# Kernel optimization log

Measured on AMD Instinct MI355X. Metric: run time of the kernel, lower is better.

## Reference

```python
import jax, jax.numpy as jnp
import numpy as np

B, S, H, NREL = 4, 512, 256, 99


def setup_inputs() -> dict:
    key = jax.random.key(0)
    ks = jax.random.split(key, 6)
    return {
        "queries": jax.random.normal(ks[0], (B, S, H), dtype=jnp.float32),
        "keys": jax.random.normal(ks[1], (B, S, H), dtype=jnp.float32),
        "relations": jax.random.randint(ks[2], (B, S, S), 0, NREL, dtype=jnp.int64),
        "Wq": jax.random.normal(ks[3], (H, H), dtype=jnp.float32) * 0.02,
        "bq": jnp.zeros((H,), dtype=jnp.float32),
        "Wk": jax.random.normal(ks[4], (H, H), dtype=jnp.float32) * 0.02,
        "bk": jnp.zeros((H,), dtype=jnp.float32),
        "rel_emb": jax.random.normal(ks[5], (NREL, H), dtype=jnp.float32) * 0.02,
    }


def reference(queries, keys, relations, Wq, bq, Wk, bk, rel_emb):
    # Linear projections (torch Linear: x @ W.T + b)
    q = queries @ Wq.T + bq        # [B, Sq, H]
    k = keys @ Wk.T + bk           # [B, Sk, H]
    r = rel_emb[relations]         # [B, Sq, Sk, H]

    # single head: qk^T + q . r^T, scaled
    qk = jnp.einsum("bqd,bkd->bqk", q, k)       # [B, Sq, Sk]
    qr = jnp.einsum("bqd,bqkd->bqk", q, r)      # [B, Sq, Sk]
    scale = 1.0 / jnp.sqrt(jnp.asarray(q.shape[-1], q.dtype))
    logits = (qk + qr) * scale
    return jax.nn.softmax(logits, axis=-1)       # squeezed head dim -> [B, Sq, Sk]
```

## Files before the change

kernel.cpp:

```cpp
#include <hip/hip_runtime.h>

typedef __attribute__((ext_vector_type(8))) short bf8;
typedef __attribute__((ext_vector_type(4))) float f4;

#define QBF  0
#define KBF  524288
#define WQBF 1048576
#define WKBF 1114112
#define REBF 1179648

static __device__ __forceinline__ short bfr(float x) {
    union { float f; unsigned u; } v; v.f = x;
    return (short)((v.u + 0x7FFF + ((v.u >> 16) & 1)) >> 16);
}
static __device__ __forceinline__ bf8 pack8(float4 a, float4 b) {
    bf8 r;
    r[0] = bfr(a.x); r[1] = bfr(a.y); r[2] = bfr(a.z); r[3] = bfr(a.w);
    r[4] = bfr(b.x); r[5] = bfr(b.y); r[6] = bfr(b.z); r[7] = bfr(b.w);
    return r;
}

__global__ __launch_bounds__(256) void cast_kernel(const float* __restrict__ Wq,
                                                   const float* __restrict__ Wk,
                                                   const float* __restrict__ re,
                                                   short* __restrict__ ws) {
    int e8 = (blockIdx.x * 256 + threadIdx.x) * 8;
    float4 a = make_float4(0.f, 0.f, 0.f, 0.f), b = a;
    short* dst;
    if (e8 < 65536) {
        const float4* s = (const float4*)(Wq + e8);
        a = s[0]; b = s[1];
        dst = ws + WQBF + e8;
    } else if (e8 < 131072) {
        const float4* s = (const float4*)(Wk + (e8 - 65536));
        a = s[0]; b = s[1];
        dst = ws + WKBF + (e8 - 65536);
    } else {
        int idx = e8 - 131072;
        dst = ws + REBF + idx;
        if ((idx >> 8) < 99) {
            const float4* s = (const float4*)(re + idx);
            a = s[0]; b = s[1];
        }
    }
    *(bf8*)dst = pack8(a, b);
}

__global__ __launch_bounds__(512) void proj_kernel(const float* __restrict__ queries,
                                                   const float* __restrict__ keys,
                                                   const float* __restrict__ bq,
                                                   const float* __restrict__ bk,
                                                   short* __restrict__ ws) {
    int mat = blockIdx.x >> 6;
    int t = blockIdx.x & 63;
    int m0 = (t >> 2) * 128;
    int n0 = (t & 3) * 64;
    int w = threadIdx.x >> 6;
    int lane = threadIdx.x & 63;
    int n15 = lane & 15, quad = lane >> 4;

    const float* x = mat ? keys : queries;
    const short* wb = ws + (mat ? WKBF : WQBF);
    const float* bias = mat ? bk : bq;
    short* outp = ws + (mat ? KBF : QBF);

    int mrow = m0 + w * 16 + n15;
    bf8 afr[8];
#pragma unroll
    for (int kk = 0; kk < 8; kk++) {
        const float4* ap = (const float4*)(x + mrow * 256 + kk * 32 + quad * 8);
        afr[kk] = pack8(ap[0], ap[1]);
    }

    f4 z = {0.f, 0.f, 0.f, 0.f};
    f4 c[4] = {z, z, z, z};
#pragma unroll
    for (int nt = 0; nt < 4; nt++) {
        int col = n0 + nt * 16 + n15;
        const short* wr = wb + col * 256 + quad * 8;
#pragma unroll
        for (int kk = 0; kk < 8; kk++) {
            bf8 bfrag = *(const bf8*)(wr + kk * 32);
            c[nt] = __builtin_amdgcn_mfma_f32_16x16x32_bf16(afr[kk], bfrag, c[nt], 0, 0, 0);
        }
    }

    int mbase = m0 + w * 16 + quad * 4;
#pragma unroll
    for (int nt = 0; nt < 4; nt++) {
        int col = n0 + nt * 16 + n15;
        float bv = bias[col];
#pragma unroll
        for (int reg = 0; reg < 4; reg++)
            outp[(mbase + reg) * 256 + col] = bfr(c[nt][reg] + bv);
    }
}

__global__ __launch_bounds__(512) void attn_kernel(const int* __restrict__ relations,
                                                   const short* __restrict__ ws,
                                                   float* __restrict__ out) {
    __shared__ float qr_l[16][112];
    __shared__ float red_m[16][8];
    __shared__ float red_s[16][8];

    int b = blockIdx.x >> 5;
    int i0 = (blockIdx.x & 31) * 16;
    int gi0 = b * 512 + i0;
    int w = threadIdx.x >> 6;
    int lane = threadIdx.x & 63;
    int n15 = lane & 15, quad = lane >> 4;
    int j0 = w * 64;

    const int* rb = relations + (gi0 + quad * 4) * 512 + j0 + n15;
    int rv[4][4];
#pragma unroll
    for (int reg = 0; reg < 4; reg++)
#pragma unroll
        for (int nt = 0; nt < 4; nt++)
            rv[nt][reg] = rb[reg * 512 + nt * 16];

    const short* qbf = ws + QBF;
    const short* kbf = ws + KBF;
    const short* rebf = ws + REBF;

    int arow = gi0 + n15;
    bf8 afr[8];
#pragma unroll
    for (int kk = 0; kk < 8; kk++)
        afr[kk] = *(const bf8*)(qbf + arow * 256 + kk * 32 + quad * 8);

    f4 z = {0.f, 0.f, 0.f, 0.f};
    f4 c[4] = {z, z, z, z};
#pragma unroll
    for (int nt = 0; nt < 4; nt++) {
        int krow = b * 512 + j0 + nt * 16 + n15;
        const short* kr = kbf + krow * 256 + quad * 8;
#pragma unroll
        for (int kk = 0; kk < 8; kk++) {
            bf8 bfrag = *(const bf8*)(kr + kk * 32);
            c[nt] = __builtin_amdgcn_mfma_f32_16x16x32_bf16(afr[kk], bfrag, c[nt], 0, 0, 0);
        }
    }

    if (w < 7) {
        f4 cq = z;
        const short* rr = rebf + (w * 16 + n15) * 256 + quad * 8;
#pragma unroll
        for (int kk = 0; kk < 8; kk++) {
            bf8 bfrag = *(const bf8*)(rr + kk * 32);
            cq = __builtin_amdgcn_mfma_f32_16x16x32_bf16(afr[kk], bfrag, cq, 0, 0, 0);
        }
#pragma unroll
        for (int reg = 0; reg < 4; reg++)
            qr_l[quad * 4 + reg][w * 16 + n15] = cq[reg];
    }
    __syncthreads();

    const float scale = 0.0625f;
    float lg[4][4];
#pragma unroll
    for (int nt = 0; nt < 4; nt++)
#pragma unroll
        for (int reg = 0; reg < 4; reg++)
            lg[nt][reg] = (c[nt][reg] + qr_l[quad * 4 + reg][rv[nt][reg]]) * scale;

    float pm[4];
#pragma unroll
    for (int reg = 0; reg < 4; reg++) {
        float m = fmaxf(fmaxf(lg[0][reg], lg[1][reg]), fmaxf(lg[2][reg], lg[3][reg]));
#pragma unroll
        for (int d = 1; d <= 8; d <<= 1) m = fmaxf(m, __shfl_xor(m, d, 64));
        pm[reg] = m;
    }
    if (n15 == 0)
#pragma unroll
        for (int reg = 0; reg < 4; reg++) red_m[quad * 4 + reg][w] = pm[reg];
    __syncthreads();
    float M[4];
#pragma unroll
    for (int reg = 0; reg < 4; reg++) {
        f4 a0 = *(const f4*)&red_m[quad * 4 + reg][0];
        f4 a1 = *(const f4*)&red_m[quad * 4 + reg][4];
        M[reg] = fmaxf(fmaxf(fmaxf(a0[0], a0[1]), fmaxf(a0[2], a0[3])),
                       fmaxf(fmaxf(a1[0], a1[1]), fmaxf(a1[2], a1[3])));
    }

    float ps[4];
#pragma unroll
    for (int reg = 0; reg < 4; reg++) {
        float s = 0.f;
#pragma unroll
        for (int nt = 0; nt < 4; nt++) {
            float e = __expf(lg[nt][reg] - M[reg]);
            lg[nt][reg] = e;
            s += e;
        }
#pragma unroll
        for (int d = 1; d <= 8; d <<= 1) s += __shfl_xor(s, d, 64);
        ps[reg] = s;
    }
    if (n15 == 0)
#pragma unroll
        for (int reg = 0; reg < 4; reg++) red_s[quad * 4 + reg][w] = ps[reg];
    __syncthreads();
    float inv[4];
#pragma unroll
    for (int reg = 0; reg < 4; reg++) {
        f4 a0 = *(const f4*)&red_s[quad * 4 + reg][0];
        f4 a1 = *(const f4*)&red_s[quad * 4 + reg][4];
        inv[reg] = 1.f / (a0[0] + a0[1] + a0[2] + a0[3] + a1[0] + a1[1] + a1[2] + a1[3]);
    }

    float* ob = out + (gi0 + quad * 4) * 512 + j0 + n15;
#pragma unroll
    for (int reg = 0; reg < 4; reg++)
#pragma unroll
        for (int nt = 0; nt < 4; nt++)
            ob[reg * 512 + nt * 16] = lg[nt][reg] * inv[reg];
}

extern "C" void kernel_launch(void* const* d_in, const int* in_sizes, int n_in,
                              void* d_out, int out_size, void* d_ws, size_t ws_size,
                              hipStream_t stream) {
    const float* queries = (const float*)d_in[0];
    const float* keys = (const float*)d_in[1];
    const int* relations = (const int*)d_in[2];
    const float* Wq = (const float*)d_in[3];
    const float* bq = (const float*)d_in[4];
    const float* Wk = (const float*)d_in[5];
    const float* bk = (const float*)d_in[6];
    const float* rel_emb = (const float*)d_in[7];
    short* wss = (short*)d_ws;
    float* out = (float*)d_out;

    hipLaunchKernelGGL(cast_kernel, dim3(78), dim3(256), 0, stream, Wq, Wk, rel_emb, wss);
    hipLaunchKernelGGL(proj_kernel, dim3(128), dim3(512), 0, stream, queries, keys, bq, bk, wss);
    hipLaunchKernelGGL(attn_kernel, dim3(128), dim3(512), 0, stream, relations, wss, out);
}
```

Baseline: 99.82 us.

## Fuse cast, projection and attention into one cooperative kernel with grid sync

Merges the three launches into one cooperative kernel of 135 blocks. Blocks 0-127 convert their weight slice to bf16 straight into LDS and compute the Q/K projections, while blocks 128-134 convert the relation embeddings. After a grid-wide sync, the first 128 blocks run the attention and softmax. The relations index loads are issued before the projection so their latency overlaps it. This removes two kernel launch gaps and the round trip of the bf16 weights through global memory, at the cost of a grid barrier and cooperative launch overhead.

```diff
diff --git a/kernel.cpp b/kernel.cpp
--- a/kernel.cpp
+++ b/kernel.cpp
@@ -1,13 +1,14 @@
 #include <hip/hip_runtime.h>
+#include <hip/hip_cooperative_groups.h>
+
+namespace cg = cooperative_groups;
 
 typedef __attribute__((ext_vector_type(8))) short bf8;
 typedef __attribute__((ext_vector_type(4))) float f4;
 
 #define QBF  0
 #define KBF  524288
-#define WQBF 1048576
-#define WKBF 1114112
-#define REBF 1179648
+#define REBF 1048576
 
 static __device__ __forceinline__ short bfr(float x) {
     union { float f; unsigned u; } v; v.f = x;
@@ -20,104 +21,110 @@
     return r;
 }
 
-__global__ __launch_bounds__(256) void cast_kernel(const float* __restrict__ Wq,
-                                                   const float* __restrict__ Wk,
-                                                   const float* __restrict__ re,
-                                                   short* __restrict__ ws) {
-    int e8 = (blockIdx.x * 256 + threadIdx.x) * 8;
-    float4 a = make_float4(0.f, 0.f, 0.f, 0.f), b = a;
-    short* dst;
-    if (e8 < 65536) {
-        const float4* s = (const float4*)(Wq + e8);
-        a = s[0]; b = s[1];
-        dst = ws + WQBF + e8;
-    } else if (e8 < 131072) {
-        const float4* s = (const float4*)(Wk + (e8 - 65536));
-        a = s[0]; b = s[1];
-        dst = ws + WKBF + (e8 - 65536);
+__global__ __launch_bounds__(512) void fused_kernel(const int* __restrict__ relations,
+                                                    const float* __restrict__ queries,
+                                                    const float* __restrict__ keys,
+                                                    const float* __restrict__ bq,
+                                                    const float* __restrict__ bk,
+                                                    const float* __restrict__ Wq,
+                                                    const float* __restrict__ Wk,
+                                                    const float* __restrict__ rel_emb,
+                                                    short* __restrict__ ws,
+                                                    float* __restrict__ out) {
+    __shared__ union {
+        short w_l[64 * 264];
+        struct {
+            float qr[16][112];
+            float rm[16][8];
+            float rs[16][8];
+        } p1;
+    } sm;
+
+    cg::grid_group grid = cg::this_grid();
+
+    int blk = blockIdx.x;
+    int tid = threadIdx.x;
+    int w = tid >> 6;
+    int lane = tid & 63;
+    int n15 = lane & 15, quad = lane >> 4;
+
+    int rv[4][4];
+    if (blk < 128) {
+        int b_ = blk >> 5;
+        int i0_ = (blk & 31) * 16;
+        const int* rb = relations + ((b_ * 512 + i0_) + quad * 4) * 512 + w * 64 + n15;
+#pragma unroll
+        for (int reg = 0; reg < 4; reg++)
+#pragma unroll
+            for (int nt = 0; nt < 4; nt++)
+                rv[nt][reg] = rb[reg * 512 + nt * 16];
+    }
+
+    if (blk < 128) {
+        int mat = blk >> 6;
+        int t = blk & 63;
+        int m0 = (t >> 2) * 128;
+        int n0 = (t & 3) * 64;
+        const float* x = mat ? keys : queries;
+        const float* W = mat ? Wk : Wq;
+        const float* bias = mat ? bk : bq;
+        short* outp = ws + (mat ? KBF : QBF);
+
+#pragma unroll
+        for (int cc = 0; cc < 4; cc++) {
+            int chunk = cc * 512 + tid;
+            int row = chunk >> 5, col8 = chunk & 31;
+            const float4* s = (const float4*)(W + (n0 + row) * 256 + col8 * 8);
+            *(bf8*)&sm.w_l[row * 264 + col8 * 8] = pack8(s[0], s[1]);
+        }
+
+        int mrow = m0 + w * 16 + n15;
+        bf8 afr[8];
+#pragma unroll
+        for (int kk = 0; kk < 8; kk++) {
+            const float4* ap = (const float4*)(x + mrow * 256 + kk * 32 + quad * 8);
+            afr[kk] = pack8(ap[0], ap[1]);
+        }
+        __syncthreads();
+
+        f4 z = {0.f, 0.f, 0.f, 0.f};
+        f4 c[4] = {z, z, z, z};
+#pragma unroll
+        for (int nt = 0; nt < 4; nt++) {
+            const short* wr = &sm.w_l[(nt * 16 + n15) * 264 + quad * 8];
+#pragma unroll
+            for (int kk = 0; kk < 8; kk++) {
+                bf8 bfrag = *(const bf8*)(wr + kk * 32);
+                c[nt] = __builtin_amdgcn_mfma_f32_16x16x32_bf16(afr[kk], bfrag, c[nt], 0, 0, 0);
+            }
+        }
+
+        int mbase = m0 + w * 16 + quad * 4;
+#pragma unroll
+        for (int nt = 0; nt < 4; nt++) {
+            int col = n0 + nt * 16 + n15;
+            float bv = bias[col];
+#pragma unroll
+            for (int reg = 0; reg < 4; reg++)
+                outp[(mbase + reg) * 256 + col] = bfr(c[nt][reg] + bv);
+        }
     } else {
-        int idx = e8 - 131072;
-        dst = ws + REBF + idx;
-        if ((idx >> 8) < 99) {
-            const float4* s = (const float4*)(re + idx);
+        int idx8 = ((blk - 128) * 512 + tid) * 8;
+        float4 a = make_float4(0.f, 0.f, 0.f, 0.f), b = a;
+        if ((idx8 >> 8) < 99) {
+            const float4* s = (const float4*)(rel_emb + idx8);
             a = s[0]; b = s[1];
         }
-    }
-    *(bf8*)dst = pack8(a, b);
-}
-
-__global__ __launch_bounds__(512) void proj_kernel(const float* __restrict__ queries,
-                                                   const float* __restrict__ keys,
-                                                   const float* __restrict__ bq,
-                                                   const float* __restrict__ bk,
-                                                   short* __restrict__ ws) {
-    int mat = blockIdx.x >> 6;
-    int t = blockIdx.x & 63;
-    int m0 = (t >> 2) * 128;
-    int n0 = (t & 3) * 64;
-    int w = threadIdx.x >> 6;
-    int lane = threadIdx.x & 63;
-    int n15 = lane & 15, quad = lane >> 4;
-
-    const float* x = mat ? keys : queries;
-    const short* wb = ws + (mat ? WKBF : WQBF);
-    const float* bias = mat ? bk : bq;
-    short* outp = ws + (mat ? KBF : QBF);
-
-    int mrow = m0 + w * 16 + n15;
-    bf8 afr[8];
-#pragma unroll
-    for (int kk = 0; kk < 8; kk++) {
-        const float4* ap = (const float4*)(x + mrow * 256 + kk * 32 + quad * 8);
-        afr[kk] = pack8(ap[0], ap[1]);
-    }
-
-    f4 z = {0.f, 0.f, 0.f, 0.f};
-    f4 c[4] = {z, z, z, z};
-#pragma unroll
-    for (int nt = 0; nt < 4; nt++) {
-        int col = n0 + nt * 16 + n15;
-        const short* wr = wb + col * 256 + quad * 8;
-#pragma unroll
-        for (int kk = 0; kk < 8; kk++) {
-            bf8 bfrag = *(const bf8*)(wr + kk * 32);
-            c[nt] = __builtin_amdgcn_mfma_f32_16x16x32_bf16(afr[kk], bfrag, c[nt], 0, 0, 0);
-        }
-    }
-
-    int mbase = m0 + w * 16 + quad * 4;
-#pragma unroll
-    for (int nt = 0; nt < 4; nt++) {
-        int col = n0 + nt * 16 + n15;
-        float bv = bias[col];
-#pragma unroll
-        for (int reg = 0; reg < 4; reg++)
-            outp[(mbase + reg) * 256 + col] = bfr(c[nt][reg] + bv);
-    }
-}
-
-__global__ __launch_bounds__(512) void attn_kernel(const int* __restrict__ relations,
-                                                   const short* __restrict__ ws,
-                                                   float* __restrict__ out) {
-    __shared__ float qr_l[16][112];
-    __shared__ float red_m[16][8];
-    __shared__ float red_s[16][8];
-
-    int b = blockIdx.x >> 5;
-    int i0 = (blockIdx.x & 31) * 16;
+        *(bf8*)(ws + REBF + idx8) = pack8(a, b);
+    }
+
+    grid.sync();
+    if (blk >= 128) return;
+
+    int b = blk >> 5;
+    int i0 = (blk & 31) * 16;
     int gi0 = b * 512 + i0;
-    int w = threadIdx.x >> 6;
-    int lane = threadIdx.x & 63;
-    int n15 = lane & 15, quad = lane >> 4;
     int j0 = w * 64;
-
-    const int* rb = relations + (gi0 + quad * 4) * 512 + j0 + n15;
-    int rv[4][4];
-#pragma unroll
-    for (int reg = 0; reg < 4; reg++)
-#pragma unroll
-        for (int nt = 0; nt < 4; nt++)
-            rv[nt][reg] = rb[reg * 512 + nt * 16];
 
     const short* qbf = ws + QBF;
     const short* kbf = ws + KBF;
@@ -152,7 +159,7 @@
         }
 #pragma unroll
         for (int reg = 0; reg < 4; reg++)
-            qr_l[quad * 4 + reg][w * 16 + n15] = cq[reg];
+            sm.p1.qr[quad * 4 + reg][w * 16 + n15] = cq[reg];
     }
     __syncthreads();
 
@@ -162,7 +169,7 @@
     for (int nt = 0; nt < 4; nt++)
 #pragma unroll
         for (int reg = 0; reg < 4; reg++)
-            lg[nt][reg] = (c[nt][reg] + qr_l[quad * 4 + reg][rv[nt][reg]]) * scale;
+            lg[nt][reg] = (c[nt][reg] + sm.p1.qr[quad * 4 + reg][rv[nt][reg]]) * scale;
 
     float pm[4];
 #pragma unroll
@@ -174,13 +181,13 @@
     }
     if (n15 == 0)
 #pragma unroll
-        for (int reg = 0; reg < 4; reg++) red_m[quad * 4 + reg][w] = pm[reg];
+        for (int reg = 0; reg < 4; reg++) sm.p1.rm[quad * 4 + reg][w] = pm[reg];
     __syncthreads();
     float M[4];
 #pragma unroll
     for (int reg = 0; reg < 4; reg++) {
-        f4 a0 = *(const f4*)&red_m[quad * 4 + reg][0];
-        f4 a1 = *(const f4*)&red_m[quad * 4 + reg][4];
+        f4 a0 = *(const f4*)&sm.p1.rm[quad * 4 + reg][0];
+        f4 a1 = *(const f4*)&sm.p1.rm[quad * 4 + reg][4];
         M[reg] = fmaxf(fmaxf(fmaxf(a0[0], a0[1]), fmaxf(a0[2], a0[3])),
                        fmaxf(fmaxf(a1[0], a1[1]), fmaxf(a1[2], a1[3])));
     }
@@ -201,13 +208,13 @@
     }
     if (n15 == 0)
 #pragma unroll
-        for (int reg = 0; reg < 4; reg++) red_s[quad * 4 + reg][w] = ps[reg];
+        for (int reg = 0; reg < 4; reg++) sm.p1.rs[quad * 4 + reg][w] = ps[reg];
     __syncthreads();
     float inv[4];
 #pragma unroll
     for (int reg = 0; reg < 4; reg++) {
-        f4 a0 = *(const f4*)&red_s[quad * 4 + reg][0];
-        f4 a1 = *(const f4*)&red_s[quad * 4 + reg][4];
+        f4 a0 = *(const f4*)&sm.p1.rs[quad * 4 + reg][0];
+        f4 a1 = *(const f4*)&sm.p1.rs[quad * 4 + reg][4];
         inv[reg] = 1.f / (a0[0] + a0[1] + a0[2] + a0[3] + a1[0] + a1[1] + a1[2] + a1[3]);
     }
 
@@ -233,7 +240,8 @@
     short* wss = (short*)d_ws;
     float* out = (float*)d_out;
 
-    hipLaunchKernelGGL(cast_kernel, dim3(78), dim3(256), 0, stream, Wq, Wk, rel_emb, wss);
-    hipLaunchKernelGGL(proj_kernel, dim3(128), dim3(512), 0, stream, queries, keys, bq, bk, wss);
-    hipLaunchKernelGGL(attn_kernel, dim3(128), dim3(512), 0, stream, relations, wss, out);
-}
+    void* kargs[] = {(void*)&relations, (void*)&queries, (void*)&keys,
+                     (void*)&bq, (void*)&bk, (void*)&Wq, (void*)&Wk,
+                     (void*)&rel_emb, (void*)&wss, (void*)&out};
+    hipLaunchCooperativeKernel((void*)fused_kernel, dim3(135), dim3(512), kargs, 0, stream);
+}
```

After: 130.8 us. 31.0% more time.

## Fold weight casting into projection kernel and double attention grid parallelism

Applied to the files above, without the earlier changes.

Removes the separate cast kernel: projection blocks now load and convert their weight tile to bf16 in shared memory, and extra blocks cast rel_emb. The projection grid grows to 256 smaller-row tiles, and the attention kernel processes 8 query rows per block (256 blocks) with duplicated MFMA rows, writing only half. This cuts one launch and spreads work over more CUs, at the cost of redundant MFMA work and repeated weight conversion per block.

```diff
diff --git a/kernel.cpp b/kernel.cpp
--- a/kernel.cpp
+++ b/kernel.cpp
@@ -5,9 +5,7 @@
 
 #define QBF  0
 #define KBF  524288
-#define WQBF 1048576
-#define WKBF 1114112
-#define REBF 1179648
+#define REBF 1048576
 
 static __device__ __forceinline__ short bfr(float x) {
     union { float f; unsigned u; } v; v.f = x;
@@ -20,49 +18,50 @@
     return r;
 }
 
-__global__ __launch_bounds__(256) void cast_kernel(const float* __restrict__ Wq,
-                                                   const float* __restrict__ Wk,
-                                                   const float* __restrict__ re,
-                                                   short* __restrict__ ws) {
-    int e8 = (blockIdx.x * 256 + threadIdx.x) * 8;
-    float4 a = make_float4(0.f, 0.f, 0.f, 0.f), b = a;
-    short* dst;
-    if (e8 < 65536) {
-        const float4* s = (const float4*)(Wq + e8);
-        a = s[0]; b = s[1];
-        dst = ws + WQBF + e8;
-    } else if (e8 < 131072) {
-        const float4* s = (const float4*)(Wk + (e8 - 65536));
-        a = s[0]; b = s[1];
-        dst = ws + WKBF + (e8 - 65536);
-    } else {
-        int idx = e8 - 131072;
-        dst = ws + REBF + idx;
-        if ((idx >> 8) < 99) {
-            const float4* s = (const float4*)(re + idx);
-            a = s[0]; b = s[1];
-        }
-    }
-    *(bf8*)dst = pack8(a, b);
-}
-
-__global__ __launch_bounds__(512) void proj_kernel(const float* __restrict__ queries,
+__global__ __launch_bounds__(256) void proj_kernel(const float* __restrict__ queries,
                                                    const float* __restrict__ keys,
                                                    const float* __restrict__ bq,
                                                    const float* __restrict__ bk,
+                                                   const float* __restrict__ Wq,
+                                                   const float* __restrict__ Wk,
+                                                   const float* __restrict__ rel_emb,
                                                    short* __restrict__ ws) {
-    int mat = blockIdx.x >> 6;
-    int t = blockIdx.x & 63;
-    int m0 = (t >> 2) * 128;
+    __shared__ short w_l[64 * 264];
+    int blk = blockIdx.x;
+    int tid = threadIdx.x;
+
+    if (blk >= 256) {
+        int idx = ((blk - 256) * 256 + tid) * 16;
+        float4 a = make_float4(0.f, 0.f, 0.f, 0.f), b = a, c = a, d = a;
+        if ((idx >> 8) < 99) {
+            const float4* s = (const float4*)(rel_emb + idx);
+            a = s[0]; b = s[1]; c = s[2]; d = s[3];
+        }
+        *(bf8*)(ws + REBF + idx) = pack8(a, b);
+        *(bf8*)(ws + REBF + idx + 8) = pack8(c, d);
+        return;
+    }
+
+    int mat = blk >> 7;
+    int t = blk & 127;
+    int m0 = (t >> 2) * 64;
     int n0 = (t & 3) * 64;
-    int w = threadIdx.x >> 6;
-    int lane = threadIdx.x & 63;
-    int n15 = lane & 15, quad = lane >> 4;
-
     const float* x = mat ? keys : queries;
-    const short* wb = ws + (mat ? WKBF : WQBF);
+    const float* W = mat ? Wk : Wq;
     const float* bias = mat ? bk : bq;
     short* outp = ws + (mat ? KBF : QBF);
+
+    int w = tid >> 6;
+    int lane = tid & 63;
+    int n15 = lane & 15, quad = lane >> 4;
+
+#pragma unroll
+    for (int cc = 0; cc < 8; cc++) {
+        int chunk = cc * 256 + tid;
+        int row = chunk >> 5, col8 = chunk & 31;
+        const float4* s = (const float4*)(W + (n0 + row) * 256 + col8 * 8);
+        *(bf8*)&w_l[row * 264 + col8 * 8] = pack8(s[0], s[1]);
+    }
 
     int mrow = m0 + w * 16 + n15;
     bf8 afr[8];
@@ -71,13 +70,13 @@
         const float4* ap = (const float4*)(x + mrow * 256 + kk * 32 + quad * 8);
         afr[kk] = pack8(ap[0], ap[1]);
     }
+    __syncthreads();
 
     f4 z = {0.f, 0.f, 0.f, 0.f};
     f4 c[4] = {z, z, z, z};
 #pragma unroll
     for (int nt = 0; nt < 4; nt++) {
-        int col = n0 + nt * 16 + n15;
-        const short* wr = wb + col * 256 + quad * 8;
+        const short* wr = &w_l[(nt * 16 + n15) * 264 + quad * 8];
 #pragma unroll
         for (int kk = 0; kk < 8; kk++) {
             bf8 bfrag = *(const bf8*)(wr + kk * 32);
@@ -103,15 +102,16 @@
     __shared__ float red_m[16][8];
     __shared__ float red_s[16][8];
 
-    int b = blockIdx.x >> 5;
-    int i0 = (blockIdx.x & 31) * 16;
+    int blk = blockIdx.x;
+    int b = blk >> 6;
+    int i0 = (blk & 63) * 8;
     int gi0 = b * 512 + i0;
     int w = threadIdx.x >> 6;
     int lane = threadIdx.x & 63;
     int n15 = lane & 15, quad = lane >> 4;
     int j0 = w * 64;
 
-    const int* rb = relations + (gi0 + quad * 4) * 512 + j0 + n15;
+    const int* rb = relations + (gi0 + (quad & 1) * 4) * 512 + j0 + n15;
     int rv[4][4];
 #pragma unroll
     for (int reg = 0; reg < 4; reg++)
@@ -123,7 +123,7 @@
     const short* kbf = ws + KBF;
     const short* rebf = ws + REBF;
 
-    int arow = gi0 + n15;
+    int arow = gi0 + (n15 & 7);
     bf8 afr[8];
 #pragma unroll
     for (int kk = 0; kk < 8; kk++)
@@ -211,12 +211,14 @@
         inv[reg] = 1.f / (a0[0] + a0[1] + a0[2] + a0[3] + a1[0] + a1[1] + a1[2] + a1[3]);
     }
 
-    float* ob = out + (gi0 + quad * 4) * 512 + j0 + n15;
-#pragma unroll
-    for (int reg = 0; reg < 4; reg++)
-#pragma unroll
-        for (int nt = 0; nt < 4; nt++)
-            ob[reg * 512 + nt * 16] = lg[nt][reg] * inv[reg];
+    if (quad < 2) {
+        float* ob = out + (gi0 + quad * 4) * 512 + j0 + n15;
+#pragma unroll
+        for (int reg = 0; reg < 4; reg++)
+#pragma unroll
+            for (int nt = 0; nt < 4; nt++)
+                ob[reg * 512 + nt * 16] = lg[nt][reg] * inv[reg];
+    }
 }
 
 extern "C" void kernel_launch(void* const* d_in, const int* in_sizes, int n_in,
@@ -233,7 +235,7 @@
     short* wss = (short*)d_ws;
     float* out = (float*)d_out;
 
-    hipLaunchKernelGGL(cast_kernel, dim3(78), dim3(256), 0, stream, Wq, Wk, rel_emb, wss);
-    hipLaunchKernelGGL(proj_kernel, dim3(128), dim3(512), 0, stream, queries, keys, bq, bk, wss);
-    hipLaunchKernelGGL(attn_kernel, dim3(128), dim3(512), 0, stream, relations, wss, out);
-}
+    hipLaunchKernelGGL(proj_kernel, dim3(263), dim3(256), 0, stream,
+                       queries, keys, bq, bk, Wq, Wk, rel_emb, wss);
+    hipLaunchKernelGGL(attn_kernel, dim3(256), dim3(512), 0, stream, relations, wss, out);
+}
```

Result: faster. 90.97 us, median of 2 (-8.9%).
